# Kernel tuning notes

Measured on AMD Instinct MI355X. Metric: run time of the kernel, lower is better.

## Reference

```python
import jax, jax.numpy as jnp
import numpy as np

B, S, D_IN, D_OUT = 4, 2048, 768, 768

def setup_inputs() -> dict:
    key = jax.random.key(0)
    kx, kq, kk, kv = jax.random.split(key, 4)
    scale = 1.0 / np.sqrt(D_IN)
    return {
        "x": jax.random.normal(kx, (B, S, D_IN), dtype=jnp.float32),
        "Wq": jax.random.normal(kq, (D_OUT, D_IN), dtype=jnp.float32) * scale,
        "Wk": jax.random.normal(kk, (D_OUT, D_IN), dtype=jnp.float32) * scale,
        "Wv": jax.random.normal(kv, (D_OUT, D_IN), dtype=jnp.float32) * scale,
    }

def reference(x, Wq, Wk, Wv):
    # torch Linear: y = x @ W.T  (W is [d_out, d_in])
    q = jnp.einsum('bsd,od->bso', x, Wq)
    k = jnp.einsum('bsd,od->bso', x, Wk)
    v = jnp.einsum('bsd,od->bso', x, Wv)
    scores = jnp.einsum('bqo,bko->bqk', q, k)  # [B,S,S]
    causal = jnp.tril(jnp.ones((scores.shape[1], scores.shape[2]), dtype=bool))
    neg_inf = jnp.array(-jnp.inf, dtype=scores.dtype)
    scores = jnp.where(causal, scores, neg_inf)
    inv_sqrt_d = jnp.asarray(1.0 / np.sqrt(q.shape[-1]), dtype=scores.dtype)
    weights = jax.nn.softmax(scores * inv_sqrt_d, axis=-1)
    # dropout p=0.0 -> identity
    return jnp.einsum('bqk,bko->bqo', weights, v)
```

## Files before the change

### kernel.cpp

```cpp
#include <hip/hip_runtime.h>
#include <hip/hip_bf16.h>
#include <cstdint>
#include <cstddef>


typedef __attribute__((ext_vector_type(8))) short short8;
typedef __attribute__((ext_vector_type(4))) float f32x4;

#define GPTR(p) (const __attribute__((address_space(1))) void*)(p)
#define LPTR(p) (__attribute__((address_space(3))) void*)(p)

constexpr int CB = 4, CS = 2048, CD = 768;
constexpr int CBS = CB * CS;

__device__ inline unsigned short f2bf_bits(float v) {
    __hip_bfloat16 h = __float2bfloat16(v);
    unsigned short u;
    __builtin_memcpy(&u, &h, 2);
    return u;
}

__device__ inline ushort4 cvt4(float4 f) {
    ushort4 u;
    u.x = f2bf_bits(f.x); u.y = f2bf_bits(f.y);
    u.z = f2bf_bits(f.z); u.w = f2bf_bits(f.w);
    return u;
}

__global__ __launch_bounds__(256) void cvt_all(
    const float4* __restrict__ x,  const float4* __restrict__ wq,
    const float4* __restrict__ wk, const float4* __restrict__ wv,
    ushort4* __restrict__ x16, ushort4* __restrict__ w16,
    float4* __restrict__ rsum4)
{
    constexpr int NX = CBS * CD / 4;
    constexpr int NW = CD * CD / 4;
    constexpr int NT = NX + 3 * NW;
    const int i = blockIdx.x * 256 + threadIdx.x;
    if (i < NX) {
        x16[i] = cvt4(x[i]);
    } else if (i < NT) {
        const int j = i - NX;
        if (j < NW)            w16[j] = cvt4(wq[j]);
        else if (j < 2 * NW)   w16[j] = cvt4(wk[j - NW]);
        else                   w16[j] = cvt4(wv[j - 2 * NW]);
    } else {
        const int j = i - NT;
        rsum4[j] = float4{0.f, 0.f, 0.f, 0.f};
    }
}

template <int BM>
__device__ __forceinline__ void gemm_core(
    const __hip_bfloat16* __restrict__ A,
    const __hip_bfloat16* __restrict__ B,
    __hip_bfloat16* As, __hip_bfloat16* Bs,
    int m0, int n0, int K, int kend,
    f32x4 (&acc)[BM / 32][4])
{
    constexpr int AC = BM / 16;
    constexpr int SC = AC + 8;
    constexpr int MI = BM / 32;

    const int t  = threadIdx.x;
    const int w  = t >> 6;
    const int l  = t & 63;
    const int lq = l >> 4;
    const int lm = l & 15;
    const int wm = (w >> 1) * (BM / 2);
    const int wn = (w & 1) * 64;

    const int srow = l >> 2;
    const int scol = (l & 3) * 8;

    for (int k0 = 0; k0 < kend; k0 += 64) {
        __syncthreads();
#pragma unroll
        for (int ci = 0; ci < 2 * SC / 4; ++ci) {
            const int c    = ci * 4 + w;
            const int slab = (c >= SC) ? 1 : 0;
            const int cc   = c - slab * SC;
            const int kofs = k0 + slab * 32 + scol;
            if (cc < AC) {
                __builtin_amdgcn_global_load_lds(
                    GPTR(A + (size_t)(m0 + cc * 16 + srow) * K + kofs),
                    LPTR(&As[slab * BM * 32 + cc * 512]), 16, 0, 0);
            } else {
                const int c2 = cc - AC;
                __builtin_amdgcn_global_load_lds(
                    GPTR(B + (size_t)(n0 + c2 * 16 + srow) * K + kofs),
                    LPTR(&Bs[slab * 128 * 32 + c2 * 512]), 16, 0, 0);
            }
        }
        __syncthreads();

#pragma unroll
        for (int kk = 0; kk < 2; ++kk) {
            short8 af[MI], bf[4];
#pragma unroll
            for (int i = 0; i < MI; ++i)
                af[i] = *(const short8*)&As[kk * BM * 32 + (wm + i * 16 + lm) * 32 + lq * 8];
#pragma unroll
            for (int j = 0; j < 4; ++j)
                bf[j] = *(const short8*)&Bs[kk * 128 * 32 + (wn + j * 16 + lm) * 32 + lq * 8];

#pragma unroll
            for (int i = 0; i < MI; ++i)
#pragma unroll
                for (int j = 0; j < 4; ++j)
                    acc[i][j] = __builtin_amdgcn_mfma_f32_16x16x32_bf16(
                        af[i], bf[j], acc[i][j], 0, 0, 0);
        }
    }
}

template <int MI>
__device__ __forceinline__ void zero_acc(f32x4 (&acc)[MI][4]) {
#pragma unroll
    for (int i = 0; i < MI; ++i)
#pragma unroll
        for (int j = 0; j < 4; ++j)
            acc[i][j] = f32x4{0.f, 0.f, 0.f, 0.f};
}

__global__ __launch_bounds__(256) void qkv_gemm(
    const __hip_bfloat16* __restrict__ x16,
    const __hip_bfloat16* __restrict__ w16,
    __hip_bfloat16* __restrict__ q16,
    __hip_bfloat16* __restrict__ k16,
    __hip_bfloat16* __restrict__ vt16)
{
    __shared__ __align__(16) __hip_bfloat16 As[2 * 128 * 32];
    __shared__ __align__(16) __hip_bfloat16 Bs[2 * 128 * 32];

    const int t  = threadIdx.x;
    const int w  = t >> 6;
    const int l  = t & 63;
    const int lq = l >> 4;
    const int lm = l & 15;
    const int wm = (w >> 1) * 64;
    const int wn = (w & 1) * 64;

    f32x4 acc[4][4];
    zero_acc<4>(acc);

    const __hip_bfloat16* A;
    const __hip_bfloat16* B;
    __hip_bfloat16* C;
    int m0, n0, ldc;

    const int id = blockIdx.x;
    if (id < 768) {
        const int proj = id / 384;
        const int r    = id % 384;
        n0 = (r % 6) * 128;
        m0 = (r / 6) * 128;
        A = x16; B = w16 + (size_t)proj * CD * CD;
        C = proj ? k16 : q16; ldc = CD;
    } else {
        int r = id - 768;
        const int b  = r / 96;  r %= 96;
        n0 = (r % 16) * 128;
        m0 = (r / 16) * 128;
        A = w16 + (size_t)2 * CD * CD;
        B = x16  + (size_t)b * CS * CD;
        C = vt16 + (size_t)b * CD * CS; ldc = CS;
    }

    gemm_core<128>(A, B, As, Bs, m0, n0, CD, CD, acc);

#pragma unroll
    for (int i = 0; i < 4; ++i)
#pragma unroll
        for (int j = 0; j < 4; ++j) {
            const int n = n0 + wn + j * 16 + lm;
#pragma unroll
            for (int r = 0; r < 4; ++r) {
                const int m = m0 + wm + i * 16 + lq * 4 + r;
                C[(size_t)m * ldc + n] = __float2bfloat16(acc[i][j][r]);
            }
        }
}

__global__ __launch_bounds__(256) void scores_gemm(
    const __hip_bfloat16* __restrict__ q16,
    const __hip_bfloat16* __restrict__ k16,
    __hip_bfloat16* __restrict__ sp16,
    float* __restrict__ rowsum,
    float scale)
{
    const int g  = blockIdx.x;
    const int b  = g & 3;
    const int tt = g >> 2;
    int s = (int)sqrtf((float)tt);
    while ((s + 1) * (s + 1) <= tt) ++s;
    while (s * s > tt) --s;
    int mi, nj;
    if (tt < s * (s + 1)) { mi = 2 * s - 1; nj = tt - s * s; }
    else                  { mi = 2 * s;     nj = tt - s * (s + 1); }
    const int m0 = mi * 64;
    const int n0 = nj * 128;

    __shared__ __align__(16) __hip_bfloat16 As[2 * 64 * 32];
    __shared__ __align__(16) __hip_bfloat16 Bs[2 * 128 * 32];

    const __hip_bfloat16* A = q16 + (size_t)b * CS * CD;
    const __hip_bfloat16* B = k16 + (size_t)b * CS * CD;
    __hip_bfloat16* C = sp16 + (size_t)b * CS * CS;
    float* rs = rowsum + (size_t)b * CS;

    f32x4 acc[2][4];
    zero_acc<2>(acc);
    gemm_core<64>(A, B, As, Bs, m0, n0, CD, CD, acc);

    const int t  = threadIdx.x;
    const int w  = t >> 6;
    const int l  = t & 63;
    const int lq = l >> 4;
    const int lm = l & 15;
    const int wm = (w >> 1) * 32;
    const int wn = (w & 1) * 64;

#pragma unroll
    for (int i = 0; i < 2; ++i) {
        float psum[4] = {0.f, 0.f, 0.f, 0.f};
#pragma unroll
        for (int j = 0; j < 4; ++j) {
            const int n = n0 + wn + j * 16 + lm;
#pragma unroll
            for (int r = 0; r < 4; ++r) {
                const int m = m0 + wm + i * 16 + lq * 4 + r;
                float e = (n <= m) ? __expf(acc[i][j][r] * scale) : 0.f;
                C[(size_t)m * CS + n] = __float2bfloat16(e);
                psum[r] += e;
            }
        }
#pragma unroll
        for (int r = 0; r < 4; ++r) {
#pragma unroll
            for (int off = 1; off < 16; off <<= 1)
                psum[r] += __shfl_xor(psum[r], off);
            if (lm == 0) {
                const int m = m0 + wm + i * 16 + lq * 4 + r;
                atomicAdd(&rs[m], psum[r]);
            }
        }
    }
}

__global__ __launch_bounds__(256) void pv_gemm(
    const __hip_bfloat16* __restrict__ sp16,
    const __hip_bfloat16* __restrict__ vt16,
    const float* __restrict__ rowsum,
    float* __restrict__ out)
{
    const int id   = blockIdx.x;
    const int mrev = id / 24;
    int r          = id % 24;
    const int b    = r / 6;
    const int n0   = (r % 6) * 128;
    const int mi   = 31 - mrev;
    const int m0   = mi * 64;
    const int kend = m0 + 64;

    __shared__ __align__(16) __hip_bfloat16 As[2 * 64 * 32];
    __shared__ __align__(16) __hip_bfloat16 Bs[2 * 128 * 32];

    const __hip_bfloat16* A = sp16 + (size_t)b * CS * CS;
    const __hip_bfloat16* B = vt16 + (size_t)b * CD * CS;
    float* Co = out + (size_t)b * CS * CD;
    const float* rs = rowsum + (size_t)b * CS;

    f32x4 acc[2][4];
    zero_acc<2>(acc);
    gemm_core<64>(A, B, As, Bs, m0, n0, CS, kend, acc);

    const int t  = threadIdx.x;
    const int w  = t >> 6;
    const int l  = t & 63;
    const int lq = l >> 4;
    const int lm = l & 15;
    const int wm = (w >> 1) * 32;
    const int wn = (w & 1) * 64;

#pragma unroll
    for (int i = 0; i < 2; ++i) {
        float inv[4];
#pragma unroll
        for (int r2 = 0; r2 < 4; ++r2)
            inv[r2] = 1.0f / rs[m0 + wm + i * 16 + lq * 4 + r2];
#pragma unroll
        for (int j = 0; j < 4; ++j) {
            const int n = n0 + wn + j * 16 + lm;
#pragma unroll
            for (int r2 = 0; r2 < 4; ++r2) {
                const int m = m0 + wm + i * 16 + lq * 4 + r2;
                Co[(size_t)m * CD + n] = acc[i][j][r2] * inv[r2];
            }
        }
    }
}

extern "C" void kernel_launch(void* const* d_in, const int* in_sizes, int n_in,
                              void* d_out, int out_size, void* d_ws, size_t ws_size,
                              hipStream_t stream)
{
    const float* x  = (const float*)d_in[0];
    const float* Wq = (const float*)d_in[1];
    const float* Wk = (const float*)d_in[2];
    const float* Wv = (const float*)d_in[3];
    float* out = (float*)d_out;

    char* ws = (char*)d_ws;
    size_t off = 0;
    auto alloc = [&](size_t bytes) { char* p = ws + off; off += bytes; return p; };

    __hip_bfloat16* x16  = (__hip_bfloat16*)alloc((size_t)CBS * CD * 2);
    __hip_bfloat16* q16  = (__hip_bfloat16*)alloc((size_t)CBS * CD * 2);
    __hip_bfloat16* k16  = (__hip_bfloat16*)alloc((size_t)CBS * CD * 2);
    __hip_bfloat16* vt16 = (__hip_bfloat16*)alloc((size_t)CBS * CD * 2);
    __hip_bfloat16* sp16 = (__hip_bfloat16*)alloc((size_t)CB * CS * CS * 2);
    __hip_bfloat16* w16  = (__hip_bfloat16*)alloc((size_t)3 * CD * CD * 2);
    float*          rsum = (float*)alloc((size_t)CB * CS * sizeof(float));

    constexpr int NCVT_BLK = (CBS * CD + 3 * CD * CD) / 4 / 256 + 8;
    cvt_all<<<NCVT_BLK, 256, 0, stream>>>(
        (const float4*)x, (const float4*)Wq, (const float4*)Wk, (const float4*)Wv,
        (ushort4*)x16, (ushort4*)w16, (float4*)rsum);

    qkv_gemm<<<1152, 256, 0, stream>>>(x16, w16, q16, k16, vt16);

    scores_gemm<<<1088, 256, 0, stream>>>(
        q16, k16, sp16, rsum, 0.03608439182435161f);

    pv_gemm<<<768, 256, 0, stream>>>(sp16, vt16, rsum, out);
}
```

Measured before the change: 186.3 us.

## Double-buffer GEMM LDS tiles to overlap global loads with MFMA

```diff
diff --git a/kernel.cpp b/kernel.cpp
--- a/kernel.cpp
+++ b/kernel.cpp
@@ -73,44 +73,49 @@
     const int srow = l >> 2;
     const int scol = (l & 3) * 8;
 
-    for (int k0 = 0; k0 < kend; k0 += 64) {
+    auto stage = [&](int buf, int k0) {
+#pragma unroll
+        for (int ci = 0; ci < SC / 4; ++ci) {
+            const int c = ci * 4 + w;
+            if (c < AC) {
+                __builtin_amdgcn_global_load_lds(
+                    GPTR(A + (size_t)(m0 + c * 16 + srow) * K + k0 + scol),
+                    LPTR(&As[buf * BM * 32 + c * 512]), 16, 0, 0);
+            } else {
+                const int c2 = c - AC;
+                __builtin_amdgcn_global_load_lds(
+                    GPTR(B + (size_t)(n0 + c2 * 16 + srow) * K + k0 + scol),
+                    LPTR(&Bs[buf * 128 * 32 + c2 * 512]), 16, 0, 0);
+            }
+        }
+    };
+
+    stage(0, 0);
+    asm volatile("s_waitcnt vmcnt(0)");
+    __syncthreads();
+
+    int cur = 0;
+    for (int k0 = 0; k0 < kend; k0 += 32) {
+        if (k0 + 32 < kend)
+            stage(cur ^ 1, k0 + 32);
+
+        short8 af[MI], bf[4];
+#pragma unroll
+        for (int i = 0; i < MI; ++i)
+            af[i] = *(const short8*)&As[cur * BM * 32 + (wm + i * 16 + lm) * 32 + lq * 8];
+#pragma unroll
+        for (int j = 0; j < 4; ++j)
+            bf[j] = *(const short8*)&Bs[cur * 128 * 32 + (wn + j * 16 + lm) * 32 + lq * 8];
+
+#pragma unroll
+        for (int i = 0; i < MI; ++i)
+#pragma unroll
+            for (int j = 0; j < 4; ++j)
+                acc[i][j] = __builtin_amdgcn_mfma_f32_16x16x32_bf16(
+                    af[i], bf[j], acc[i][j], 0, 0, 0);
+
         __syncthreads();
-#pragma unroll
-        for (int ci = 0; ci < 2 * SC / 4; ++ci) {
-            const int c    = ci * 4 + w;
-            const int slab = (c >= SC) ? 1 : 0;
-            const int cc   = c - slab * SC;
-            const int kofs = k0 + slab * 32 + scol;
-            if (cc < AC) {
-                __builtin_amdgcn_global_load_lds(
-                    GPTR(A + (size_t)(m0 + cc * 16 + srow) * K + kofs),
-                    LPTR(&As[slab * BM * 32 + cc * 512]), 16, 0, 0);
-            } else {
-                const int c2 = cc - AC;
-                __builtin_amdgcn_global_load_lds(
-                    GPTR(B + (size_t)(n0 + c2 * 16 + srow) * K + kofs),
-                    LPTR(&Bs[slab * 128 * 32 + c2 * 512]), 16, 0, 0);
-            }
-        }
-        __syncthreads();
-
-#pragma unroll
-        for (int kk = 0; kk < 2; ++kk) {
-            short8 af[MI], bf[4];
-#pragma unroll
-            for (int i = 0; i < MI; ++i)
-                af[i] = *(const short8*)&As[kk * BM * 32 + (wm + i * 16 + lm) * 32 + lq * 8];
-#pragma unroll
-            for (int j = 0; j < 4; ++j)
-                bf[j] = *(const short8*)&Bs[kk * 128 * 32 + (wn + j * 16 + lm) * 32 + lq * 8];
-
-#pragma unroll
-            for (int i = 0; i < MI; ++i)
-#pragma unroll
-                for (int j = 0; j < 4; ++j)
-                    acc[i][j] = __builtin_amdgcn_mfma_f32_16x16x32_bf16(
-                        af[i], bf[j], acc[i][j], 0, 0, 0);
-        }
+        cur ^= 1;
     }
 }
 
```

Result: slower. 193.9 us (+4.0%).
